# Kernel tuning notes

Hardware: AMD Instinct MI355X
Metric: run time of the kernel (lower is better)

The kernel has to match this reference:

```python
import jax, jax.numpy as jnp
import numpy as np

NUM_SEG = 196  # fixed max number of segments (fill_max of segment ids)


def setup_inputs() -> dict:
    key = jax.random.key(0)
    ks = jax.random.split(key, 6)
    B, H, W = 16, 224, 224
    in_chans, inter_dim, embed_dim, k = 3, 64, 768, 7
    x = jax.random.normal(ks[0], (B, in_chans, H, W), jnp.float32)
    segment = jax.random.randint(ks[1], (B, H, W), 0, NUM_SEG, dtype=jnp.int64)
    conv1_w = jax.random.normal(ks[2], (inter_dim, in_chans, k, k), jnp.float32) * 0.02
    conv1_b = jnp.zeros((inter_dim,), jnp.float32)
    pos_embed = jax.random.normal(ks[3], (1, inter_dim, H, W), jnp.float32) * 0.02
    conv2_w = jax.random.normal(ks[4], (embed_dim, inter_dim, 3), jnp.float32) * 0.02
    conv2_b = jnp.zeros((embed_dim,), jnp.float32)
    return {"x": x, "segment": segment, "conv1_w": conv1_w, "conv1_b": conv1_b,
            "pos_embed": pos_embed, "conv2_w": conv2_w, "conv2_b": conv2_b}


def _remap(s):
    # torch.unique(return_inverse=True): map ids to ranks in sorted unique order.
    present = jnp.zeros((NUM_SEG,), jnp.int32).at[s].set(1)
    rank = jnp.cumsum(present) - 1  # rank of each possible id among present ids
    return rank[s]


def _segment_mean(hc, idx):
    # hc: [C, N], idx: [N] -> [C, NUM_SEG]; empty segments -> 0 (sum 0 / clamp 1)
    sums = jax.ops.segment_sum(hc.T, idx, num_segments=NUM_SEG)           # [S, C]
    cnt = jax.ops.segment_sum(jnp.ones(idx.shape, hc.dtype), idx,
                              num_segments=NUM_SEG)                       # [S]
    return (sums / jnp.maximum(cnt, 1.0)[:, None]).T


def reference(x, segment, conv1_w, conv1_b, pos_embed, conv2_w, conv2_b):
    # conv1, stride 1, 'same' padding (odd kernel -> SAME matches torch)
    h = jax.lax.conv_general_dilated(
        x, conv1_w, window_strides=(1, 1), padding='SAME',
        dimension_numbers=('NCHW', 'OIHW', 'NCHW')) + conv1_b[None, :, None, None]
    h = h + pos_embed
    B, C, H, W = h.shape
    # segment already at (H, W): nearest-interpolate to same size is identity
    seg = segment.reshape(B, -1).astype(jnp.int32)      # [B, H*W]
    f_segment = jax.vmap(_remap)(seg)                   # per-sample unique inverse
    pooled = jax.vmap(_segment_mean)(h.reshape(B, C, -1), f_segment)  # [B, C, S]
    # conv1d k=3, padding=1
    out = jax.lax.conv_general_dilated(
        pooled, conv2_w, window_strides=(1,), padding=[(1, 1)],
        dimension_numbers=('NCH', 'OIH', 'NCH')) + conv2_b[None, :, None]
    out = out.transpose(0, 2, 1)                        # [B, S, embed_dim]
    return out, f_segment.reshape(B, 1, H, W)
```

## Files before the change

### kernel.cpp

```cpp
#include <hip/hip_runtime.h>
#include <hip/hip_bf16.h>

constexpr int B = 16, H = 224, W = 224, CI = 3, CO = 64, K = 7;
constexpr int SEG = 196, E = 768;
constexpr int HW = H * W;
constexpr int PP = 201;
constexpr int EC = 32;

constexpr int TSLOTS = 10;

typedef __attribute__((ext_vector_type(8))) short bf16x8;
typedef __attribute__((ext_vector_type(16))) float f32x16;

__device__ inline unsigned short bfb(float f) {
    union { __hip_bfloat16 h; unsigned short u; } cv; cv.h = __float2bfloat16(f); return cv.u;
}
__device__ inline unsigned pack2(float lo, float hi) {
    return (unsigned)bfb(lo) | ((unsigned)bfb(hi) << 16);
}
__device__ inline float bf2f(unsigned short u) {
    return __uint_as_float(((unsigned)u) << 16);
}

__global__ void k_count(const int* __restrict__ seg, int* __restrict__ present,
                        unsigned* __restrict__ counts_raw) {
    __shared__ unsigned cnt[SEG];
    const int tid = threadIdx.x, b = blockIdx.y, y0 = blockIdx.x * 8;
    for (int i = tid; i < SEG; i += 256) cnt[i] = 0u;
    __syncthreads();
    for (int i = tid; i < 8 * W; i += 256) {
        int s = seg[b * HW + y0 * W + i];
        present[b * SEG + s] = 1;
        atomicAdd(&cnt[s], 1u);
    }
    __syncthreads();
    for (int i = tid; i < SEG; i += 256)
        if (cnt[i]) atomicAdd(&counts_raw[b * SEG + i], cnt[i]);
}

__global__ void k_offsets(const int* __restrict__ present,
                          const unsigned* __restrict__ counts_raw,
                          int* __restrict__ rank, int* __restrict__ off_rank,
                          int* __restrict__ cnt_rank, unsigned* __restrict__ cursor) {
    __shared__ int buf[256];
    const int b = blockIdx.x, t = threadIdx.x;
    int pres = (t < SEG) ? present[b * SEG + t] : 0;
    int cv   = (t < SEG) ? (int)counts_raw[b * SEG + t] : 0;
    buf[t] = pres; __syncthreads();
    for (int off = 1; off < 256; off <<= 1) {
        int u = (t >= off) ? buf[t - off] : 0; __syncthreads();
        buf[t] += u; __syncthreads();
    }
    int rk = buf[t] - 1;
    if (t < SEG) rank[b * SEG + t] = rk;
    __syncthreads();
    buf[t] = cv; __syncthreads();
    for (int off = 1; off < 256; off <<= 1) {
        int u = (t >= off) ? buf[t - off] : 0; __syncthreads();
        buf[t] += u; __syncthreads();
    }
    int offx = buf[t] - cv;
    if (t < SEG) {
        cursor[b * SEG + t] = (unsigned)offx;
        cnt_rank[b * SEG + t] = 0;
        off_rank[b * SEG + t] = 0;
    }
    __syncthreads();
    if (t < SEG && pres) {
        cnt_rank[b * SEG + rk] = cv;
        off_rank[b * SEG + rk] = offx;
    }
}

__global__ void k_scatter(const int* __restrict__ seg, const int* __restrict__ rank,
                          unsigned* __restrict__ cursor, unsigned* __restrict__ bucket,
                          float* __restrict__ out2) {
    __shared__ unsigned bcnt[SEG];
    __shared__ int base_l[SEG];
    __shared__ int rank_lds[SEG];
    __shared__ unsigned char ss[8 * W];
    __shared__ unsigned short lp[8 * W];
    const int tid = threadIdx.x, b = blockIdx.y, y0 = blockIdx.x * 8;
    for (int i = tid; i < SEG; i += 256) { bcnt[i] = 0u; rank_lds[i] = rank[b * SEG + i]; }
    __syncthreads();
    for (int i = tid; i < 8 * W; i += 256) {
        int s = seg[b * HW + y0 * W + i];
        ss[i] = (unsigned char)s;
        out2[b * HW + y0 * W + i] = (float)rank_lds[s];
        lp[i] = (unsigned short)atomicAdd(&bcnt[s], 1u);
    }
    __syncthreads();
    for (int i = tid; i < SEG; i += 256)
        if (bcnt[i]) base_l[i] = (int)atomicAdd(&cursor[b * SEG + i], bcnt[i]);
    __syncthreads();
    for (int i = tid; i < 8 * W; i += 256) {
        int s = ss[i];
        bucket[b * HW + base_l[s] + lp[i]] = (unsigned)(y0 * W + i);
    }
}

__global__ void k_post(const float* __restrict__ pos, const float* __restrict__ b1,
                       unsigned short* __restrict__ pos_t) {
    const int p = blockIdx.x * 256 + threadIdx.x;
    unsigned d[32];
    #pragma unroll
    for (int c = 0; c < 32; ++c) {
        float v0 = pos[(size_t)(2 * c) * HW + p]     + b1[2 * c];
        float v1 = pos[(size_t)(2 * c + 1) * HW + p] + b1[2 * c + 1];
        d[c] = pack2(v0, v1);
    }
    uint4* op = (uint4*)&pos_t[(size_t)p * 64];
    #pragma unroll
    for (int q = 0; q < 8; ++q) {
        uint4 v = {d[4 * q], d[4 * q + 1], d[4 * q + 2], d[4 * q + 3]};
        op[q] = v;
    }
}

__global__ void k_wt(const float* __restrict__ w1, unsigned short* __restrict__ w1t) {
    int i = blockIdx.x * 256 + threadIdx.x;
    if (i < 7 * 2 * 2 * 64 * 8) {
        int e = i & 7, lane = (i >> 3) & 63, cg = (i >> 9) & 1, ks = (i >> 10) & 1, ky = i >> 11;
        int kk = ks * 16 + (lane >> 5) * 8 + e;
        int co = cg * 32 + (lane & 31);
        float v = 0.f;
        if (kk < 24) {
            int ci = kk >> 3, kx = kk & 7;
            if (kx < 7) v = w1[((co * 3 + ci) * 7 + ky) * 7 + kx];
        }
        w1t[i] = bfb(v);
    }
}

__launch_bounds__(256, 3)
__global__ void k_conv_mfma(const float* __restrict__ x,
                            const unsigned short* __restrict__ w1t,
                            const unsigned short* __restrict__ pos_t,
                            __hip_bfloat16* __restrict__ h, int b0) {
    __shared__ unsigned short Tl[TSLOTS * 4 * 32 * 8];

    const int tid = threadIdx.x;
    const int lb  = blockIdx.x;
    const int b   = b0 + lb;
    const int x0  = blockIdx.y * 32;
    const int y0  = blockIdx.z * 28;
    const int lane = tid & 63;
    const int ln31 = lane & 31;
    const int g    = lane >> 5;
    const int wave = tid >> 6;
    const int wr   = wave >> 1;
    const int cg   = wave & 1;

    bf16x8 bfr[7][2];
    #pragma unroll
    for (int ky = 0; ky < 7; ++ky)
        #pragma unroll
        for (int ks = 0; ks < 2; ++ks)
            bfr[ky][ks] = *(const bf16x8*)&w1t[((((ky * 2 + ks) * 2 + cg) * 64) + lane) * 8];

    for (int i = tid; i < TSLOTS * 4 * 32 * 8; i += 256) Tl[i] = 0;
    __syncthreads();
    for (int idx = tid; idx < 96 * TSLOTS; idx += 256) {
        int jr = idx / 96, rem = idx % 96;
        int ci = rem >> 5, xl = rem & 31;
        int r = y0 - 3 + jr;
        unsigned slot = (unsigned)(r + 3) % TSLOTS;
        uint4 dv = {0, 0, 0, 0};
        if (r >= 0 && r < H) {
            const float* xr = &x[((size_t)(b * CI + ci) * H + r) * W];
            float v[7];
            #pragma unroll
            for (int kx = 0; kx < 7; ++kx) {
                int gx = x0 + xl - 3 + kx;
                v[kx] = (gx >= 0 && gx < W) ? xr[gx] : 0.f;
            }
            dv.x = pack2(v[0], v[1]); dv.y = pack2(v[2], v[3]);
            dv.z = pack2(v[4], v[5]); dv.w = pack2(v[6], 0.f);
        }
        *(uint4*)&Tl[((slot * 4 + ci) * 32 + xl) * 8] = dv;
    }
    __syncthreads();

    for (int s = 0; s < 7; ++s) {
        const int ys = y0 + s * 4;
        const int row0 = ys + wr * 2;

        float ld0[7], ld1[7];
        int slot0 = 0, slot1 = 0, ci0 = 0, ci1 = 0, xl0 = 0, xl1 = 0;
        bool act1 = false;
        if (s < 6) {
            {
                int idx = tid;
                int jr = idx / 96, rem = idx % 96;
                ci0 = rem >> 5; xl0 = rem & 31;
                int r = ys + 7 + jr;
                slot0 = (int)((unsigned)(r + 3) % TSLOTS);
                #pragma unroll
                for (int kx = 0; kx < 7; ++kx) {
                    int gx = x0 + xl0 - 3 + kx;
                    bool ok = (r < H) && gx >= 0 && gx < W;
                    ld0[kx] = ok ? x[((size_t)(b * CI + ci0) * H + r) * W + gx] : 0.f;
                }
            }
            {
                int idx = tid + 256;
                act1 = idx < 384;
                int jr = idx / 96, rem = idx % 96;
                ci1 = rem >> 5; xl1 = rem & 31;
                int r = ys + 7 + jr;
                slot1 = (int)((unsigned)(r + 3) % TSLOTS);
                #pragma unroll
                for (int kx = 0; kx < 7; ++kx) {
                    int gx = x0 + xl1 - 3 + kx;
                    bool ok = act1 && (r < H) && gx >= 0 && gx < W;
                    ld1[kx] = ok ? x[((size_t)(b * CI + ci1) * H + r) * W + gx] : 0.f;
                }
            }
        }

        f32x16 c0, c1;
        #pragma unroll
        for (int i = 0; i < 16; ++i) { c0[i] = 0.f; c1[i] = 0.f; }
        int sl = row0 % TSLOTS;
        #pragma unroll
        for (int ky = 0; ky < 7; ++ky) {
            const unsigned short* tq0 = &Tl[sl * (4 * 32 * 8)];
            int sl1 = (sl + 1 == TSLOTS) ? 0 : sl + 1;
            const unsigned short* tq1 = &Tl[sl1 * (4 * 32 * 8)];
            #pragma unroll
            for (int ks = 0; ks < 2; ++ks) {
                bf16x8 a0 = *(const bf16x8*)&tq0[((ks * 2 + g) * 32 + ln31) * 8];
                bf16x8 a1 = *(const bf16x8*)&tq1[((ks * 2 + g) * 32 + ln31) * 8];
                c0 = __builtin_amdgcn_mfma_f32_32x32x16_bf16(a0, bfr[ky][ks], c0, 0, 0, 0);
                c1 = __builtin_amdgcn_mfma_f32_32x32x16_bf16(a1, bfr[ky][ks], c1, 0, 0, 0);
            }
            sl = sl1;
        }

        #pragma unroll
        for (int reg = 0; reg < 16; ++reg) {
            int pxl = (reg & 3) + 8 * (reg >> 2) + 4 * g;
            int p0 = row0 * W + x0 + pxl;
            int p1 = p0 + W;
            float pv0 = bf2f(pos_t[(size_t)p0 * 64 + cg * 32 + ln31]);
            float pv1 = bf2f(pos_t[(size_t)p1 * 64 + cg * 32 + ln31]);
            h[((size_t)lb * HW + p0) * CO + cg * 32 + ln31] = __float2bfloat16(c0[reg] + pv0);
            h[((size_t)lb * HW + p1) * CO + cg * 32 + ln31] = __float2bfloat16(c1[reg] + pv1);
        }

        __syncthreads();
        if (s < 6) {
            {
                uint4 dv;
                dv.x = pack2(ld0[0], ld0[1]); dv.y = pack2(ld0[2], ld0[3]);
                dv.z = pack2(ld0[4], ld0[5]); dv.w = pack2(ld0[6], 0.f);
                *(uint4*)&Tl[((slot0 * 4 + ci0) * 32 + xl0) * 8] = dv;
            }
            if (act1) {
                uint4 dv;
                dv.x = pack2(ld1[0], ld1[1]); dv.y = pack2(ld1[2], ld1[3]);
                dv.z = pack2(ld1[4], ld1[5]); dv.w = pack2(ld1[6], 0.f);
                *(uint4*)&Tl[((slot1 * 4 + ci1) * 32 + xl1) * 8] = dv;
            }
        }
        __syncthreads();
    }
}

__global__ void k_gather(const __hip_bfloat16* __restrict__ h,
                         const unsigned* __restrict__ bucket,
                         const int* __restrict__ off_rank,
                         const int* __restrict__ cnt_rank,
                         float* __restrict__ pooled, int b0) {
    const int tid = threadIdx.x;
    const int wave = tid >> 6, lane = tid & 63;
    const int r = blockIdx.x * 4 + wave;
    const int lb = blockIdx.y, b = b0 + lb;
    const int n = cnt_rank[b * SEG + r];
    const int base = off_rank[b * SEG + r];
    const int ps = lane >> 3, cg = lane & 7;

    float acc[8] = {0.f, 0.f, 0.f, 0.f, 0.f, 0.f, 0.f, 0.f};
    const unsigned* bk = &bucket[b * HW + base];
    const int iters = (n + 7) >> 3;
    for (int i = 0; i < iters; ++i) {
        int idx = i * 8 + ps;
        if (idx < n) {
            unsigned p = bk[idx];
            uint4 u = *(const uint4*)&h[((size_t)lb * HW + p) * CO + cg * 8];
            acc[0] += __uint_as_float((u.x & 0xffffu) << 16);
            acc[1] += __uint_as_float(u.x & 0xffff0000u);
            acc[2] += __uint_as_float((u.y & 0xffffu) << 16);
            acc[3] += __uint_as_float(u.y & 0xffff0000u);
            acc[4] += __uint_as_float((u.z & 0xffffu) << 16);
            acc[5] += __uint_as_float(u.z & 0xffff0000u);
            acc[6] += __uint_as_float((u.w & 0xffffu) << 16);
            acc[7] += __uint_as_float(u.w & 0xffff0000u);
        }
    }
    #pragma unroll
    for (int m = 8; m < 64; m <<= 1)
        #pragma unroll
        for (int j = 0; j < 8; ++j) acc[j] += __shfl_xor(acc[j], m, 64);

    if (ps == 0) {
        float inv = (n > 0) ? 1.f / (float)n : 0.f;
        float* op = &pooled[((size_t)b * SEG + r) * CO + cg * 8];
        float4 v0 = {acc[0] * inv, acc[1] * inv, acc[2] * inv, acc[3] * inv};
        float4 v1 = {acc[4] * inv, acc[5] * inv, acc[6] * inv, acc[7] * inv};
        *(float4*)&op[0] = v0;
        *(float4*)&op[4] = v1;
    }
}

__launch_bounds__(256, 2)
__global__ void k_pool_conv1d(const float* __restrict__ pooledg,
                              const float* __restrict__ w2,
                              const float* __restrict__ b2,
                              float* __restrict__ out0) {
    __shared__ float pooled[CO * PP];
    __shared__ float w2l[192 * (EC + 1)];
    const int tid = threadIdx.x;
    const int b  = blockIdx.y;
    const int e0 = blockIdx.x * EC;

    for (int i = tid; i < SEG * CO; i += 256) {
        int s = i >> 6, c = i & 63;
        pooled[c * PP + s + 1] = pooledg[((size_t)b * SEG + s) * CO + c];
    }
    for (int i = tid; i < CO * 5; i += 256) {
        int c = i / 5, hh = i % 5;
        pooled[c * PP + (hh == 0 ? 0 : 196 + hh)] = 0.f;
    }
    for (int i = tid; i < EC * 192; i += 256) {
        int e = i / 192, k = i % 192;
        w2l[k * (EC + 1) + e] = w2[(size_t)(e0 + e) * 192 + k];
    }
    __syncthreads();

    const int txs = tid & 31;
    const int te  = tid >> 5;
    const int s0  = txs * 7;
    float acc[7][4];
    #pragma unroll
    for (int ss = 0; ss < 7; ++ss)
        #pragma unroll
        for (int ee = 0; ee < 4; ++ee) acc[ss][ee] = b2[e0 + te * 4 + ee];

    if (s0 < SEG) {
        #pragma unroll 4
        for (int c = 0; c < CO; ++c) {
            float pv[9];
            #pragma unroll
            for (int j = 0; j < 9; ++j) pv[j] = pooled[c * PP + s0 + j];
            #pragma unroll
            for (int dk = 0; dk < 3; ++dk) {
                float wv[4];
                #pragma unroll
                for (int ee = 0; ee < 4; ++ee)
                    wv[ee] = w2l[(c * 3 + dk) * (EC + 1) + te * 4 + ee];
                #pragma unroll
                for (int ss = 0; ss < 7; ++ss)
                    #pragma unroll
                    for (int ee = 0; ee < 4; ++ee)
                        acc[ss][ee] = fmaf(pv[ss + dk], wv[ee], acc[ss][ee]);
            }
        }
        #pragma unroll
        for (int ss = 0; ss < 7; ++ss) {
            int s = s0 + ss;
            float* op = &out0[((size_t)(b * SEG + s) * E) + e0 + te * 4];
            float4 v0 = {acc[ss][0], acc[ss][1], acc[ss][2], acc[ss][3]};
            *(float4*)op = v0;
        }
    }
}

extern "C" void kernel_launch(void* const* d_in, const int* in_sizes, int n_in,
                              void* d_out, int out_size, void* d_ws, size_t ws_size,
                              hipStream_t stream) {
    const float* x   = (const float*)d_in[0];
    const int*   seg = (const int*)d_in[1];
    const float* w1  = (const float*)d_in[2];
    const float* b1  = (const float*)d_in[3];
    const float* pos = (const float*)d_in[4];
    const float* w2  = (const float*)d_in[5];
    const float* b2  = (const float*)d_in[6];

    float* out0 = (float*)d_out;
    float* out2 = out0 + (size_t)B * SEG * E;

    int*      present    = (int*)d_ws;
    unsigned* counts_raw = (unsigned*)(present + B * SEG);
    int*      rank       = (int*)(counts_raw + B * SEG);
    int*      off_rank   = rank + B * SEG;
    int*      cnt_rank   = off_rank + B * SEG;
    unsigned* cursor     = (unsigned*)(cnt_rank + B * SEG);
    float*    pooled     = (float*)(cursor + B * SEG);
    unsigned* bucket     = (unsigned*)(pooled + (size_t)B * SEG * CO);
    unsigned short* pos_t = (unsigned short*)(bucket + (size_t)B * HW);
    unsigned short* w1t  = pos_t + (size_t)HW * CO;
    __hip_bfloat16* hbuf = (__hip_bfloat16*)(w1t + 7 * 2 * 2 * 64 * 8);

    hipMemsetAsync(d_ws, 0, (size_t)2 * B * SEG * 4, stream);

    k_post   <<<dim3(HW / 256), 256, 0, stream>>>(pos, b1, pos_t);
    k_wt     <<<dim3(56),       256, 0, stream>>>(w1, w1t);
    k_count  <<<dim3(28, B), 256, 0, stream>>>(seg, present, counts_raw);
    k_offsets<<<dim3(B),     256, 0, stream>>>(present, counts_raw, rank, off_rank, cnt_rank, cursor);
    k_scatter<<<dim3(28, B), 256, 0, stream>>>(seg, rank, cursor, bucket, out2);

    size_t used = (char*)hbuf - (char*)d_ws;
    size_t h_per_img = (size_t)HW * CO * sizeof(__hip_bfloat16);
    size_t avail = (ws_size > used) ? ws_size - used : 0;
    int ipc = (int)(avail / h_per_img);
    if (ipc < 1) ipc = 1;
    if (ipc > B) ipc = B;

    for (int b0 = 0; b0 < B; b0 += ipc) {
        int nb = (b0 + ipc <= B) ? ipc : (B - b0);
        k_conv_mfma<<<dim3(nb, 7, 8), 256, 0, stream>>>(x, w1t, pos_t, hbuf, b0);
        k_gather   <<<dim3(49, nb),   256, 0, stream>>>(hbuf, bucket, off_rank, cnt_rank, pooled, b0);
    }
    k_pool_conv1d<<<dim3(24, B), 256, 0, stream>>>(pooled, w2, b2, out0);
}
```

Before: 275.4 us.

## Split conv blocks into 4-row tiles and unroll gather loads by two

The conv kernel previously had each block walk 28 rows through a rotating 10-slot shared ring, prefetching upcoming rows between syncs. Each block now computes only 4 output rows from a one-shot 10-row halo load, so there are 7x more blocks, no ring rotation and no in-loop barriers. Only the zero-padded channel lanes are cleared instead of the whole tile. The price is re-reading the 6-row halo for every 4 output rows, which adds global and LDS traffic. The gather loop also issues two independent bucket and h loads per iteration to raise memory-level parallelism.

```diff
diff --git a/kernel.cpp b/kernel.cpp
--- a/kernel.cpp
+++ b/kernel.cpp
@@ -143,7 +143,7 @@
     const int lb  = blockIdx.x;
     const int b   = b0 + lb;
     const int x0  = blockIdx.y * 32;
-    const int y0  = blockIdx.z * 28;
+    const int y0  = blockIdx.z * 4;
     const int lane = tid & 63;
     const int ln31 = lane & 31;
     const int g    = lane >> 5;
@@ -158,13 +158,15 @@
         for (int ks = 0; ks < 2; ++ks)
             bfr[ky][ks] = *(const bf16x8*)&w1t[((((ky * 2 + ks) * 2 + cg) * 64) + lane) * 8];
 
-    for (int i = tid; i < TSLOTS * 4 * 32 * 8; i += 256) Tl[i] = 0;
-    __syncthreads();
+    for (int i = tid; i < TSLOTS * 32; i += 256) {
+        int slot = i >> 5, xl = i & 31;
+        uint4 z = {0, 0, 0, 0};
+        *(uint4*)&Tl[((slot * 4 + 3) * 32 + xl) * 8] = z;
+    }
     for (int idx = tid; idx < 96 * TSLOTS; idx += 256) {
-        int jr = idx / 96, rem = idx % 96;
+        int slot = idx / 96, rem = idx % 96;
         int ci = rem >> 5, xl = rem & 31;
-        int r = y0 - 3 + jr;
-        unsigned slot = (unsigned)(r + 3) % TSLOTS;
+        int r = y0 - 3 + slot;
         uint4 dv = {0, 0, 0, 0};
         if (r >= 0 && r < H) {
             const float* xr = &x[((size_t)(b * CI + ci) * H + r) * W];
@@ -181,89 +183,32 @@
     }
     __syncthreads();
 
-    for (int s = 0; s < 7; ++s) {
-        const int ys = y0 + s * 4;
-        const int row0 = ys + wr * 2;
-
-        float ld0[7], ld1[7];
-        int slot0 = 0, slot1 = 0, ci0 = 0, ci1 = 0, xl0 = 0, xl1 = 0;
-        bool act1 = false;
-        if (s < 6) {
-            {
-                int idx = tid;
-                int jr = idx / 96, rem = idx % 96;
-                ci0 = rem >> 5; xl0 = rem & 31;
-                int r = ys + 7 + jr;
-                slot0 = (int)((unsigned)(r + 3) % TSLOTS);
-                #pragma unroll
-                for (int kx = 0; kx < 7; ++kx) {
-                    int gx = x0 + xl0 - 3 + kx;
-                    bool ok = (r < H) && gx >= 0 && gx < W;
-                    ld0[kx] = ok ? x[((size_t)(b * CI + ci0) * H + r) * W + gx] : 0.f;
-                }
-            }
-            {
-                int idx = tid + 256;
-                act1 = idx < 384;
-                int jr = idx / 96, rem = idx % 96;
-                ci1 = rem >> 5; xl1 = rem & 31;
-                int r = ys + 7 + jr;
-                slot1 = (int)((unsigned)(r + 3) % TSLOTS);
-                #pragma unroll
-                for (int kx = 0; kx < 7; ++kx) {
-                    int gx = x0 + xl1 - 3 + kx;
-                    bool ok = act1 && (r < H) && gx >= 0 && gx < W;
-                    ld1[kx] = ok ? x[((size_t)(b * CI + ci1) * H + r) * W + gx] : 0.f;
-                }
-            }
-        }
-
-        f32x16 c0, c1;
-        #pragma unroll
-        for (int i = 0; i < 16; ++i) { c0[i] = 0.f; c1[i] = 0.f; }
-        int sl = row0 % TSLOTS;
-        #pragma unroll
-        for (int ky = 0; ky < 7; ++ky) {
-            const unsigned short* tq0 = &Tl[sl * (4 * 32 * 8)];
-            int sl1 = (sl + 1 == TSLOTS) ? 0 : sl + 1;
-            const unsigned short* tq1 = &Tl[sl1 * (4 * 32 * 8)];
-            #pragma unroll
-            for (int ks = 0; ks < 2; ++ks) {
-                bf16x8 a0 = *(const bf16x8*)&tq0[((ks * 2 + g) * 32 + ln31) * 8];
-                bf16x8 a1 = *(const bf16x8*)&tq1[((ks * 2 + g) * 32 + ln31) * 8];
-                c0 = __builtin_amdgcn_mfma_f32_32x32x16_bf16(a0, bfr[ky][ks], c0, 0, 0, 0);
-                c1 = __builtin_amdgcn_mfma_f32_32x32x16_bf16(a1, bfr[ky][ks], c1, 0, 0, 0);
-            }
-            sl = sl1;
-        }
-
-        #pragma unroll
-        for (int reg = 0; reg < 16; ++reg) {
-            int pxl = (reg & 3) + 8 * (reg >> 2) + 4 * g;
-            int p0 = row0 * W + x0 + pxl;
-            int p1 = p0 + W;
-            float pv0 = bf2f(pos_t[(size_t)p0 * 64 + cg * 32 + ln31]);
-            float pv1 = bf2f(pos_t[(size_t)p1 * 64 + cg * 32 + ln31]);
-            h[((size_t)lb * HW + p0) * CO + cg * 32 + ln31] = __float2bfloat16(c0[reg] + pv0);
-            h[((size_t)lb * HW + p1) * CO + cg * 32 + ln31] = __float2bfloat16(c1[reg] + pv1);
-        }
-
-        __syncthreads();
-        if (s < 6) {
-            {
-                uint4 dv;
-                dv.x = pack2(ld0[0], ld0[1]); dv.y = pack2(ld0[2], ld0[3]);
-                dv.z = pack2(ld0[4], ld0[5]); dv.w = pack2(ld0[6], 0.f);
-                *(uint4*)&Tl[((slot0 * 4 + ci0) * 32 + xl0) * 8] = dv;
-            }
-            if (act1) {
-                uint4 dv;
-                dv.x = pack2(ld1[0], ld1[1]); dv.y = pack2(ld1[2], ld1[3]);
-                dv.z = pack2(ld1[4], ld1[5]); dv.w = pack2(ld1[6], 0.f);
-                *(uint4*)&Tl[((slot1 * 4 + ci1) * 32 + xl1) * 8] = dv;
-            }
-        }
-        __syncthreads();
+    f32x16 c0, c1;
+    #pragma unroll
+    for (int i = 0; i < 16; ++i) { c0[i] = 0.f; c1[i] = 0.f; }
+    const int r0 = y0 + 2 * wr;
+    #pragma unroll
+    for (int ky = 0; ky < 7; ++ky) {
+        const unsigned short* tq0 = &Tl[(2 * wr + ky) * (4 * 32 * 8)];
+        const unsigned short* tq1 = &Tl[(2 * wr + ky + 1) * (4 * 32 * 8)];
+        #pragma unroll
+        for (int ks = 0; ks < 2; ++ks) {
+            bf16x8 a0 = *(const bf16x8*)&tq0[((ks * 2 + g) * 32 + ln31) * 8];
+            bf16x8 a1 = *(const bf16x8*)&tq1[((ks * 2 + g) * 32 + ln31) * 8];
+            c0 = __builtin_amdgcn_mfma_f32_32x32x16_bf16(a0, bfr[ky][ks], c0, 0, 0, 0);
+            c1 = __builtin_amdgcn_mfma_f32_32x32x16_bf16(a1, bfr[ky][ks], c1, 0, 0, 0);
+        }
+    }
+
+    #pragma unroll
+    for (int reg = 0; reg < 16; ++reg) {
+        int pxl = (reg & 3) + 8 * (reg >> 2) + 4 * g;
+        int p0 = r0 * W + x0 + pxl;
+        int p1 = p0 + W;
+        float pv0 = bf2f(pos_t[(size_t)p0 * 64 + cg * 32 + ln31]);
+        float pv1 = bf2f(pos_t[(size_t)p1 * 64 + cg * 32 + ln31]);
+        h[((size_t)lb * HW + p0) * CO + cg * 32 + ln31] = __float2bfloat16(c0[reg] + pv0);
+        h[((size_t)lb * HW + p1) * CO + cg * 32 + ln31] = __float2bfloat16(c1[reg] + pv1);
     }
 }
 
@@ -283,19 +228,26 @@
     float acc[8] = {0.f, 0.f, 0.f, 0.f, 0.f, 0.f, 0.f, 0.f};
     const unsigned* bk = &bucket[b * HW + base];
     const int iters = (n + 7) >> 3;
-    for (int i = 0; i < iters; ++i) {
-        int idx = i * 8 + ps;
-        if (idx < n) {
-            unsigned p = bk[idx];
-            uint4 u = *(const uint4*)&h[((size_t)lb * HW + p) * CO + cg * 8];
-            acc[0] += __uint_as_float((u.x & 0xffffu) << 16);
-            acc[1] += __uint_as_float(u.x & 0xffff0000u);
-            acc[2] += __uint_as_float((u.y & 0xffffu) << 16);
-            acc[3] += __uint_as_float(u.y & 0xffff0000u);
-            acc[4] += __uint_as_float((u.z & 0xffffu) << 16);
-            acc[5] += __uint_as_float(u.z & 0xffff0000u);
-            acc[6] += __uint_as_float((u.w & 0xffffu) << 16);
-            acc[7] += __uint_as_float(u.w & 0xffff0000u);
+    for (int i = 0; i < iters; i += 2) {
+        int idx0 = i * 8 + ps;
+        int idx1 = idx0 + 8;
+        uint4 u0 = {0, 0, 0, 0}, u1 = {0, 0, 0, 0};
+        if (idx0 < n) {
+            unsigned p = bk[idx0];
+            u0 = *(const uint4*)&h[((size_t)lb * HW + p) * CO + cg * 8];
+        }
+        if (idx1 < n) {
+            unsigned p = bk[idx1];
+            u1 = *(const uint4*)&h[((size_t)lb * HW + p) * CO + cg * 8];
+        }
+        const unsigned* w0 = &u0.x;
+        const unsigned* w1 = &u1.x;
+        #pragma unroll
+        for (int j = 0; j < 4; ++j) {
+            acc[2 * j]     += __uint_as_float((w0[j] & 0xffffu) << 16)
+                            + __uint_as_float((w1[j] & 0xffffu) << 16);
+            acc[2 * j + 1] += __uint_as_float(w0[j] & 0xffff0000u)
+                            + __uint_as_float(w1[j] & 0xffff0000u);
         }
     }
     #pragma unroll
@@ -419,8 +371,8 @@
 
     for (int b0 = 0; b0 < B; b0 += ipc) {
         int nb = (b0 + ipc <= B) ? ipc : (B - b0);
-        k_conv_mfma<<<dim3(nb, 7, 8), 256, 0, stream>>>(x, w1t, pos_t, hbuf, b0);
-        k_gather   <<<dim3(49, nb),   256, 0, stream>>>(hbuf, bucket, off_rank, cnt_rank, pooled, b0);
+        k_conv_mfma<<<dim3(nb, 7, 56), 256, 0, stream>>>(x, w1t, pos_t, hbuf, b0);
+        k_gather   <<<dim3(49, nb),    256, 0, stream>>>(hbuf, bucket, off_rank, cnt_rank, pooled, b0);
     }
     k_pool_conv1d<<<dim3(24, B), 256, 0, stream>>>(pooled, w2, b2, out0);
 }
```

Result: faster. 220.8 us (-19.8%).
